# Kernel optimization log

Hardware: AMD Instinct MI355X
Metric: run time of the kernel (lower is better)

The kernel has to match this reference:

```python
import jax, jax.numpy as jnp
import numpy as np

MODES = 20
WIDTH = 64
EPS = 1e-5


def spectral_conv(x, w1, w2, m1, m2):
    # x: [B, C, H, W] real; w1, w2: [Ci, Co, m1, m2, 2] (real/imag)
    B, C, H, W = x.shape
    xf = jnp.fft.rfft2(x, norm='ortho')  # [B, C, H, W//2+1] complex
    w1c = w1[..., 0] + 1j * w1[..., 1]
    w2c = w2[..., 0] + 1j * w2[..., 1]
    m1 = min(m1, H)
    m2 = min(m2, W // 2 + 1)
    top = jnp.einsum('bixy,ioxy->boxy', xf[:, :, :m1, :m2], w1c[:, :, :m1, :m2])
    bot = jnp.einsum('bixy,ioxy->boxy', xf[:, :, -m1:, :m2], w2c[:, :, :m1, :m2])
    out = jnp.zeros((B, w1.shape[1], H, W // 2 + 1), dtype=xf.dtype)
    out = out.at[:, :, :m1, :m2].set(top)
    out = out.at[:, :, H - m1:, :m2].set(bot)
    return jnp.fft.irfft2(out, s=(H, W), norm='ortho')


def batchnorm2d(x, gamma, beta):
    # training-mode BN over (B, H, W) per channel; x: [B, C, H, W]
    mean = jnp.mean(x, axis=(0, 2, 3), keepdims=True)
    var = jnp.var(x, axis=(0, 2, 3), keepdims=True)
    xn = (x - mean) * jax.lax.rsqrt(var + EPS)
    return xn * gamma[None, :, None, None] + beta[None, :, None, None]


def setup_inputs() -> dict:
    key = jax.random.key(0)
    ks = jax.random.split(key, 12)
    B, H, W, Tin2 = 8, 256, 256, 12
    scale = 1.0 / (WIDTH * WIDTH)
    return {
        'x': jax.random.normal(ks[0], (B, H, W, Tin2), jnp.float32),
        'fc0_w': jax.random.normal(ks[1], (Tin2, WIDTH), jnp.float32) * 0.1,
        'fc0_b': jnp.zeros((WIDTH,), jnp.float32),
        'sw1': scale * jax.random.normal(ks[2], (4, WIDTH, WIDTH, MODES, MODES, 2), jnp.float32),
        'sw2': scale * jax.random.normal(ks[3], (4, WIDTH, WIDTH, MODES, MODES, 2), jnp.float32),
        'cw': jax.random.normal(ks[4], (4, WIDTH, WIDTH), jnp.float32) * 0.1,
        'cb': jnp.zeros((4, WIDTH), jnp.float32),
        'bng': jnp.ones((4, WIDTH), jnp.float32),
        'bnb': jnp.zeros((4, WIDTH), jnp.float32),
        'fc1_w': jax.random.normal(ks[5], (WIDTH, 128), jnp.float32) * 0.1,
        'fc1_b': jnp.zeros((128,), jnp.float32),
        'fc2_w': jax.random.normal(ks[6], (128, 1), jnp.float32) * 0.1,
        'fc2_b': jnp.zeros((1,), jnp.float32),
    }


def reference(x, fc0_w, fc0_b, sw1, sw2, cw, cb, bng, bnb, fc1_w, fc1_b, fc2_w, fc2_b):
    # lift: [B, H, W, Tin+2] -> [B, C, H, W]
    h = jnp.einsum('bhwt,tc->bhwc', x, fc0_w) + fc0_b
    h = jnp.transpose(h, (0, 3, 1, 2))
    for l in range(4):
        spec = spectral_conv(h, sw1[l], sw2[l], MODES, MODES)
        lin = jnp.einsum('bihw,oi->bohw', h, cw[l]) + cb[l][None, :, None, None]
        h = batchnorm2d(spec + lin, bng[l], bnb[l])
        if l < 3:
            h = jax.nn.relu(h)
    h = jnp.transpose(h, (0, 2, 3, 1))  # [B, H, W, C]
    h = jax.nn.relu(jnp.einsum('bhwc,cd->bhwd', h, fc1_w) + fc1_b)
    out = jnp.einsum('bhwd,de->bhwe', h, fc2_w) + fc2_b
    return out
```

## Files before the change

### kernel.cpp

```cpp
#include <hip/hip_runtime.h>
#include <hip/hip_bf16.h>


__device__ __forceinline__ void gll16(const float* gsrc, float* ldst) {
    __builtin_amdgcn_global_load_lds(
        (const __attribute__((address_space(1))) void*)gsrc,
        (__attribute__((address_space(3))) void*)ldst, 16, 0, 0);
}

__global__ __launch_bounds__(256) void init_k(const float* __restrict__ cw,
                                              float* __restrict__ costab, float* __restrict__ sintab,
                                              float* __restrict__ EA, float* __restrict__ Tw,
                                              float* __restrict__ cwT, float* __restrict__ stats) {
    int idx = blockIdx.x * 256 + threadIdx.x;
    const float PH = 6.28318530717958647692f / 256.f;
    if (idx < 256) {
        float s, c; sincosf(idx * PH, &s, &c);
        costab[idx] = c; sintab[idx] = s;
    } else if (idx < 256 + 10240) {
        int e = idx - 256;
        int w = e / 40, n = e % 40, ky = n >> 1;
        int r = (ky * w) & 255;
        float s, c; sincosf(r * PH, &s, &c);
        EA[e] = (n & 1) ? -s : c;
    } else if (idx < 256 + 20480) {
        int e = idx - 10496;
        int kp = e >> 8, w = e & 255;
        int ky = kp >> 1, p = kp & 1;
        int r = (ky * w) & 255;
        float s, c; sincosf(r * PH, &s, &c);
        float v;
        if (ky == 0) v = p ? 0.f : (1.f / 16.f);
        else         v = p ? (-2.f / 16.f) * s : (2.f / 16.f) * c;
        Tw[e] = v;
    } else if (idx < 256 + 20480 + 16384) {
        int e = idx - 20736;
        int l = e >> 12, r2 = e & 4095;
        int i = r2 >> 6, o = r2 & 63;
        cwT[e] = cw[(l << 12) + (o << 6) + i];
    } else if (idx < 256 + 20480 + 16384 + 2048) {
        stats[idx - 37120] = 0.f;
    }
}

__global__ __launch_bounds__(256) void wtrans_k(const float* __restrict__ sw1,
                                                const float* __restrict__ sw2,
                                                unsigned int* __restrict__ wt) {
    int gid = blockIdx.x * 4 + (threadIdx.x >> 6);
    int o = threadIdx.x & 63;
    int xyc = gid % 25;
    int i = (gid / 25) & 63;
    int t2 = gid / 1600;
    const float* src = ((t2 & 1) ? sw2 : sw1) + (t2 >> 1) * 3276800;
    const float* sp = src + ((i * 64 + o) * 400 + xyc * 16) * 2;
    unsigned int* dp = wt + (size_t)(t2 * 400 + xyc * 16) * 4096 + i * 64 + o;
#pragma unroll
    for (int j = 0; j < 16; ++j) {
        float re = sp[2 * j], im = sp[2 * j + 1];
        unsigned int ur = __float_as_uint(re), ui = __float_as_uint(im);
        ur = (ur + 0x7fffu + ((ur >> 16) & 1u)) >> 16;
        ui = (ui + 0x7fffu + ((ui >> 16) & 1u)) & 0xffff0000u;
        dp[(size_t)j * 4096] = ur | ui;
    }
}

__global__ __launch_bounds__(256) void fc0_k(const float* __restrict__ x,
                                             const float* __restrict__ w,
                                             const float* __restrict__ bias,
                                             float* __restrict__ outb) {
    __shared__ float ws[768];
    __shared__ float bs[64];
    int tid = threadIdx.x;
    for (int i = tid; i < 768; i += 256) ws[i] = w[i];
    if (tid < 64) bs[tid] = bias[tid];
    __syncthreads();
    int pix = blockIdx.x * 256 + tid;
    int b = pix >> 16, hw = pix & 65535;
    float xv[12];
#pragma unroll
    for (int t = 0; t < 12; ++t) xv[t] = x[pix * 12 + t];
    int base = (b << 22) + hw;
    for (int c = 0; c < 64; ++c) {
        float a = bs[c];
#pragma unroll
        for (int t = 0; t < 12; ++t) a += xv[t] * ws[t * 64 + c];
        outb[base + (c << 16)] = a;
    }
}

__global__ __launch_bounds__(128) void dftw_k(float* __restrict__ X,
                                              const float* __restrict__ EA,
                                              float* __restrict__ T,
                                              const float* __restrict__ statsl,
                                              const float* __restrict__ g,
                                              const float* __restrict__ bt,
                                              int fuse) {
    __shared__ __align__(16) float Xs[32 * 68];
    __shared__ float Es[32 * 40];
    int tid = threadIdx.x;
    int tm = tid >> 3, tn = tid & 7;
    int row0 = blockIdx.x << 6;
    float sc = 1.f, sh = 0.f;
    if (fuse) {
        int c = (row0 >> 8) & 63;
        float ssum = statsl[c] + statsl[128 + c] + statsl[256 + c] + statsl[384 + c];
        float ssq  = statsl[64 + c] + statsl[192 + c] + statsl[320 + c] + statsl[448 + c];
        float mean = ssum * (1.f / 524288.f);
        float var = ssq * (1.f / 524288.f) - mean * mean;
        sc = g[c] * rsqrtf(var + 1e-5f);
        sh = bt[c] - mean * sc;
    }
    float acc[4][5];
#pragma unroll
    for (int i = 0; i < 4; ++i)
#pragma unroll
        for (int j = 0; j < 5; ++j) acc[i][j] = 0.f;

#pragma unroll 1
    for (int kc = 0; kc < 256; kc += 32) {
        __syncthreads();
#pragma unroll
        for (int r = 0; r < 4; ++r) {
            int m = tm + (r << 4);
            float4 v = *(const float4*)&X[(row0 + m) * 256 + kc + (tn << 2)];
            if (fuse) {
                v.x = fmaxf(fmaf(v.x, sc, sh), 0.f);
                v.y = fmaxf(fmaf(v.y, sc, sh), 0.f);
                v.z = fmaxf(fmaf(v.z, sc, sh), 0.f);
                v.w = fmaxf(fmaf(v.w, sc, sh), 0.f);
                *(float4*)&X[(row0 + m) * 256 + kc + (tn << 2)] = v;
            }
            int kb = tn << 2;
            Xs[(kb + 0) * 68 + m] = v.x;
            Xs[(kb + 1) * 68 + m] = v.y;
            Xs[(kb + 2) * 68 + m] = v.z;
            Xs[(kb + 3) * 68 + m] = v.w;
        }
        for (int i = tid; i < 1280; i += 128) Es[i] = EA[kc * 40 + i];
        __syncthreads();
#pragma unroll 4
        for (int kk = 0; kk < 32; ++kk) {
            float4 a = *(const float4*)&Xs[kk * 68 + (tm << 2)];
#pragma unroll
            for (int j = 0; j < 5; ++j) {
                float bv = Es[kk * 40 + tn * 5 + j];
                acc[0][j] += a.x * bv;
                acc[1][j] += a.y * bv;
                acc[2][j] += a.z * bv;
                acc[3][j] += a.w * bv;
            }
        }
    }
#pragma unroll
    for (int i = 0; i < 4; ++i) {
        int row = row0 + (tm << 2) + i;
#pragma unroll
        for (int j = 0; j < 5; ++j) T[row * 40 + tn * 5 + j] = acc[i][j];
    }
}

__global__ __launch_bounds__(256) void dfth_k(const float* __restrict__ T,
                                              const float* __restrict__ ct, const float* __restrict__ st,
                                              float* __restrict__ XF) {
    __shared__ __align__(16) float Ts[10240];
    __shared__ float cts[256], sts[256];
    int tid = threadIdx.x;
    int bc = blockIdx.x;
    for (int i = tid; i < 10240; i += 256) Ts[i] = T[bc * 10240 + i];
    cts[tid] = ct[tid]; sts[tid] = st[tid];
    __syncthreads();
    if (tid < 200) {
        int kxi = tid / 5, kyg = tid % 5;
        int kxa = kxi < 20 ? kxi : kxi + 216;
        float ar0 = 0, ai0 = 0, ar1 = 0, ai1 = 0, ar2 = 0, ai2 = 0, ar3 = 0, ai3 = 0;
        int r = 0;
#pragma unroll 1
        for (int h = 0; h < 256; ++h) {
            float cc = cts[r], sv = sts[r];
            r = (r + kxa) & 255;
            float4 v0 = *(const float4*)&Ts[h * 40 + (kyg << 3)];
            float4 v1 = *(const float4*)&Ts[h * 40 + (kyg << 3) + 4];
            ar0 += v0.x * cc + v0.y * sv;  ai0 += v0.y * cc - v0.x * sv;
            ar1 += v0.z * cc + v0.w * sv;  ai1 += v0.w * cc - v0.z * sv;
            ar2 += v1.x * cc + v1.y * sv;  ai2 += v1.y * cc - v1.x * sv;
            ar3 += v1.z * cc + v1.w * sv;  ai3 += v1.w * cc - v1.z * sv;
        }
        int b = bc >> 6, c = bc & 63;
        const float s = 1.f / 256.f;
        int A = (b * 40 + kxi) * 20 + (kyg << 2);
        float2* O = (float2*)XF;
        O[(A + 0) * 64 + c] = make_float2(ar0 * s, ai0 * s);
        O[(A + 1) * 64 + c] = make_float2(ar1 * s, ai1 * s);
        O[(A + 2) * 64 + c] = make_float2(ar2 * s, ai2 * s);
        O[(A + 3) * 64 + c] = make_float2(ar3 * s, ai3 * s);
    }
}

__global__ __launch_bounds__(512) void eins_t_k(const float* __restrict__ XF,
                                                const unsigned int* __restrict__ wtl,
                                                float* __restrict__ YF) {
    __shared__ float xfs[1024];
    int tid = threadIdx.x;
    int x = blockIdx.x / 20, y = blockIdx.x % 20;
    for (int i = tid; i < 1024; i += 512) {
        int b = i >> 7, rr = i & 127;
        xfs[i] = XF[(b * 40 + x) * 2560 + y * 128 + rr];
    }
    __syncthreads();
    int b = tid >> 6, o = tid & 63;
    const unsigned int* wp = wtl + (size_t)(((x < 20 ? 0 : 400) + (x % 20) * 20 + y)) * 4096 + o;
    float ar = 0.f, ai = 0.f;
#pragma unroll 8
    for (int i = 0; i < 64; ++i) {
        unsigned int wv = wp[i << 6];
        float wr = __uint_as_float(wv << 16);
        float wi = __uint_as_float(wv & 0xffff0000u);
        float xr = xfs[(b << 7) + (i << 1)];
        float xi = xfs[(b << 7) + (i << 1) + 1];
        ar += xr * wr - xi * wi;
        ai += xr * wi + xi * wr;
    }
    ((float2*)YF)[((b * 40 + x) * 20 + y) * 64 + o] = make_float2(ar, ai);
}

__global__ __launch_bounds__(512) void eins_k(const float* __restrict__ XF,
                                              const float* __restrict__ w1, const float* __restrict__ w2,
                                              float* __restrict__ YF) {
    __shared__ float xfs[1024];
    int tid = threadIdx.x;
    int x = blockIdx.x / 20, y = blockIdx.x % 20;
    for (int i = tid; i < 1024; i += 512) {
        int b = i >> 7, rr = i & 127;
        xfs[i] = XF[(b * 40 + x) * 2560 + y * 128 + rr];
    }
    __syncthreads();
    int b = tid >> 6, o = tid & 63;
    const float* wp = (x < 20) ? (w1 + (x * 20 + y) * 2) : (w2 + ((x - 20) * 20 + y) * 2);
    float ar = 0.f, ai = 0.f;
#pragma unroll 8
    for (int i = 0; i < 64; ++i) {
        float2 wv = *(const float2*)&wp[(i * 64 + o) * 800];
        float xr = xfs[(b << 7) + (i << 1)];
        float xi = xfs[(b << 7) + (i << 1) + 1];
        ar += xr * wv.x - xi * wv.y;
        ai += xr * wv.y + xi * wv.x;
    }
    ((float2*)YF)[((b * 40 + x) * 20 + y) * 64 + o] = make_float2(ar, ai);
}

__global__ __launch_bounds__(256) void idfth_k(const float* __restrict__ YF,
                                               const float* __restrict__ ct, const float* __restrict__ st,
                                               float* __restrict__ Z) {
    __shared__ __align__(16) float yfs[1600];
    __shared__ float cts[256], sts[256];
    int tid = threadIdx.x;
    int bc = blockIdx.x;
    int b = bc >> 6, co = bc & 63;
    for (int i = tid; i < 800; i += 256) {
        int kx = i / 20, ky = i % 20;
        float2 v = ((const float2*)YF)[((b * 40 + kx) * 20 + ky) * 64 + co];
        yfs[kx * 40 + 2 * ky] = v.x;
        yfs[kx * 40 + 2 * ky + 1] = v.y;
    }
    cts[tid] = ct[tid]; sts[tid] = st[tid];
    __syncthreads();
    int h = tid;
    float accr[20], acci[20];
#pragma unroll
    for (int q = 0; q < 20; ++q) { accr[q] = 0.f; acci[q] = 0.f; }
#pragma unroll 1
    for (int kxi = 0; kxi < 40; ++kxi) {
        int kxa = kxi < 20 ? kxi : kxi + 216;
        int r = (kxa * h) & 255;
        float cc = cts[r], sv = sts[r];
#pragma unroll
        for (int q = 0; q < 10; ++q) {
            float4 v = *(const float4*)&yfs[kxi * 40 + (q << 2)];
            accr[2 * q]     += v.x * cc - v.y * sv;  acci[2 * q]     += v.x * sv + v.y * cc;
            accr[2 * q + 1] += v.z * cc - v.w * sv;  acci[2 * q + 1] += v.z * sv + v.w * cc;
        }
    }
    const float s = 1.f / 16.f;
    int base = (bc * 256 + h) * 40;
#pragma unroll
    for (int q = 0; q < 10; ++q) {
        float4 o4;
        o4.x = accr[2 * q] * s;     o4.y = acci[2 * q] * s;
        o4.z = accr[2 * q + 1] * s; o4.w = acci[2 * q + 1] * s;
        *(float4*)&Z[base + (q << 2)] = o4;
    }
}

#define FMA2(I, AV, J, B4) \
    acc[I][J].x += (AV) * B4.x; acc[I][J].y += (AV) * B4.y; \
    acc[I][J].z += (AV) * B4.z; acc[I][J].w += (AV) * B4.w;

#define FMA_COL(J, B4) \
    FMA2(0, a0.x, J, B4) FMA2(1, a0.y, J, B4) FMA2(2, a0.z, J, B4) FMA2(3, a0.w, J, B4) \
    FMA2(4, a1.x, J, B4) FMA2(5, a1.y, J, B4) FMA2(6, a1.z, J, B4) FMA2(7, a1.w, J, B4)

__global__ __launch_bounds__(256, 3) void speclin_k(const float* __restrict__ hin,
                                                    const float* __restrict__ Z,
                                                    const float* __restrict__ cwTl,
                                                    const float* __restrict__ Tw,
                                                    const float* __restrict__ cbl,
                                                    float* __restrict__ pre,
                                                    float* __restrict__ statsl) {
    __shared__ __align__(16) float AZ[104 * 68];
    __shared__ __align__(16) float Bs[2][2048];
    int tid = threadIdx.x;
    int bh = blockIdx.x;
    int b = bh >> 8, h = bh & 255;
    int to = tid >> 5, tw = tid & 31;
    int o0 = to << 3;

#pragma unroll
    for (int t = 0; t < 4; ++t) {
        int i4 = tid + (t << 8);
        float4 v = *(const float4*)&cwTl[i4 << 2];
        int row = i4 >> 4, c4 = (i4 & 15) << 2;
        float* d = &AZ[row * 68 + c4];
        d[0] = v.x; d[1] = v.y; d[2] = v.z; d[3] = v.w;
    }
    {
        const float* Zrow = Z + (size_t)(((b << 6) << 8) + h) * 40;
#pragma unroll
        for (int t = 0; t < 3; ++t) {
            int i4 = tid + (t << 8);
            if (i4 < 640) {
                int q = i4 % 10, o = i4 / 10;
                float4 v = *(const float4*)&Zrow[o * 10240 + (q << 2)];
                int rb = (64 + (q << 2)) * 68 + o;
                AZ[rb] = v.x; AZ[rb + 68] = v.y; AZ[rb + 136] = v.z; AZ[rb + 204] = v.w;
            }
        }
    }
    const float* hrow = hin + ((size_t)(((b << 6) << 8) + h) << 8);
#pragma unroll
    for (int t = 0; t < 2; ++t) {
        int i4 = tid + (t << 8);
        gll16(&hrow[((i4 >> 6) << 16) + ((i4 & 63) << 2)], &Bs[0][i4 << 2]);
    }
    __syncthreads();

    float4 acc[8][2];
#pragma unroll
    for (int i = 0; i < 8; ++i) {
        acc[i][0] = make_float4(0.f, 0.f, 0.f, 0.f);
        acc[i][1] = make_float4(0.f, 0.f, 0.f, 0.f);
    }

    int cur = 0;
#pragma unroll 1
    for (int ch = 0; ch < 13; ++ch) {
        if (ch < 12) {
            int gk0 = (ch + 1) << 3;
#pragma unroll
            for (int t = 0; t < 2; ++t) {
                int i4 = tid + (t << 8);
                int kk = i4 >> 6, w4 = (i4 & 63) << 2;
                const float* src = (gk0 < 64) ? &hrow[((gk0 + kk) << 16) + w4]
                                              : &Tw[((gk0 - 64 + kk) << 8) + w4];
                gll16(src, &Bs[cur ^ 1][i4 << 2]);
            }
        }
        const float* Bc = Bs[cur];
        const float* Ac = &AZ[(ch << 3) * 68 + o0];
#pragma unroll 2
        for (int kk = 0; kk < 8; ++kk) {
            float4 a0 = *(const float4*)&Ac[kk * 68];
            float4 a1 = *(const float4*)&Ac[kk * 68 + 4];
            float4 b0 = *(const float4*)&Bc[(kk << 8) + (tw << 2)];
            float4 b1 = *(const float4*)&Bc[(kk << 8) + 128 + (tw << 2)];
            FMA_COL(0, b0)
            FMA_COL(1, b1)
        }
        __syncthreads();
        cur ^= 1;
    }

    float* srep = statsl + ((bh & 3) << 7);
#pragma unroll
    for (int i = 0; i < 8; ++i) {
        float cbv = cbl[o0 + i];
        float sum = 0.f, sq = 0.f;
        size_t obase = ((size_t)((((b << 6) + o0 + i) << 8) + h) << 8);
#pragma unroll
        for (int j = 0; j < 2; ++j) {
            float4 v = acc[i][j];
            v.x += cbv; v.y += cbv; v.z += cbv; v.w += cbv;
            *(float4*)&pre[obase + (j << 7) + (tw << 2)] = v;
            sum += v.x + v.y + v.z + v.w;
            sq  += v.x * v.x + v.y * v.y + v.z * v.z + v.w * v.w;
        }
        sum += __shfl_xor(sum, 1);  sq += __shfl_xor(sq, 1);
        sum += __shfl_xor(sum, 2);  sq += __shfl_xor(sq, 2);
        sum += __shfl_xor(sum, 4);  sq += __shfl_xor(sq, 4);
        sum += __shfl_xor(sum, 8);  sq += __shfl_xor(sq, 8);
        sum += __shfl_xor(sum, 16); sq += __shfl_xor(sq, 16);
        if ((tid & 31) == 0) {
            atomicAdd(&srep[o0 + i], sum);
            atomicAdd(&srep[64 + o0 + i], sq);
        }
    }
}

__global__ __launch_bounds__(256, 2) void fc12_k(const float* __restrict__ hin,
                                                 const float* __restrict__ statsl,
                                                 const float* __restrict__ g,
                                                 const float* __restrict__ bt,
                                                 const float* __restrict__ w1, const float* __restrict__ b1,
                                                 const float* __restrict__ w2, const float* __restrict__ b2,
                                                 float* __restrict__ out) {
    __shared__ __align__(16) float As[64 * 128];
    __shared__ __align__(16) float Bs[2][2048];
    __shared__ float scs[64], shs[64], bias2[128];
    __shared__ __align__(16) float red[4 * 256];
    int tid = threadIdx.x;
    int bh = blockIdx.x;
    int b = bh >> 8, h = bh & 255;
    int to = tid >> 4, tw = tid & 15;
    int d0 = to << 3;

    if (tid < 64) {
        float ssum = statsl[tid] + statsl[128 + tid] + statsl[256 + tid] + statsl[384 + tid];
        float ssq  = statsl[64 + tid] + statsl[192 + tid] + statsl[320 + tid] + statsl[448 + tid];
        float mean = ssum * (1.f / 524288.f);
        float var = ssq * (1.f / 524288.f) - mean * mean;
        float s = g[tid] * rsqrtf(var + 1e-5f);
        scs[tid] = s; shs[tid] = bt[tid] - mean * s;
    }
    __syncthreads();
    for (int i = tid; i < 8192; i += 256) As[i] = w1[i] * scs[i >> 7];
    if (tid < 128) {
        float a = b1[tid];
        for (int c = 0; c < 64; ++c) a += shs[c] * w1[c * 128 + tid];
        bias2[tid] = a;
    }
    const float* hrow = hin + ((size_t)(((b << 6) << 8) + h) << 8);
#pragma unroll
    for (int t = 0; t < 2; ++t) {
        int i4 = tid + (t << 8);
        gll16(&hrow[((i4 >> 6) << 16) + ((i4 & 63) << 2)], &Bs[0][i4 << 2]);
    }
    __syncthreads();

    float4 acc[8][4];
#pragma unroll
    for (int i = 0; i < 8; ++i)
#pragma unroll
        for (int j = 0; j < 4; ++j) acc[i][j] = make_float4(0.f, 0.f, 0.f, 0.f);

    int cur = 0;
#pragma unroll 1
    for (int ch = 0; ch < 8; ++ch) {
        if (ch < 7) {
#pragma unroll
            for (int t = 0; t < 2; ++t) {
                int i4 = tid + (t << 8);
                int k = i4 >> 6, w4 = (i4 & 63) << 2;
                gll16(&hrow[((((ch + 1) << 3) + k) << 16) + w4], &Bs[cur ^ 1][i4 << 2]);
            }
        }
        const float* Bc = Bs[cur];
#pragma unroll 2
        for (int kk = 0; kk < 8; ++kk) {
            int gk = (ch << 3) + kk;
            float4 a0 = *(const float4*)&As[(gk << 7) + d0];
            float4 a1 = *(const float4*)&As[(gk << 7) + d0 + 4];
            float4 b0 = *(const float4*)&Bc[(kk << 8) + (tw << 2)];
            float4 b1 = *(const float4*)&Bc[(kk << 8) + 64 + (tw << 2)];
            FMA_COL(0, b0)
            FMA_COL(1, b1)
            float4 b2 = *(const float4*)&Bc[(kk << 8) + 128 + (tw << 2)];
            float4 b3 = *(const float4*)&Bc[(kk << 8) + 192 + (tw << 2)];
            FMA_COL(2, b2)
            FMA_COL(3, b3)
        }
        __syncthreads();
        cur ^= 1;
    }

    float bb[8], wv[8];
#pragma unroll
    for (int i = 0; i < 8; ++i) { bb[i] = bias2[d0 + i]; wv[i] = w2[d0 + i]; }
    float4 p[4];
#pragma unroll
    for (int j = 0; j < 4; ++j) {
        float4 v = make_float4(0.f, 0.f, 0.f, 0.f);
#pragma unroll
        for (int i = 0; i < 8; ++i) {
            v.x += fmaxf(acc[i][j].x + bb[i], 0.f) * wv[i];
            v.y += fmaxf(acc[i][j].y + bb[i], 0.f) * wv[i];
            v.z += fmaxf(acc[i][j].z + bb[i], 0.f) * wv[i];
            v.w += fmaxf(acc[i][j].w + bb[i], 0.f) * wv[i];
        }
        v.x += __shfl_xor(v.x, 16); v.y += __shfl_xor(v.y, 16);
        v.z += __shfl_xor(v.z, 16); v.w += __shfl_xor(v.w, 16);
        v.x += __shfl_xor(v.x, 32); v.y += __shfl_xor(v.y, 32);
        v.z += __shfl_xor(v.z, 32); v.w += __shfl_xor(v.w, 32);
        p[j] = v;
    }
    int wave = tid >> 6;
    if ((tid & 63) < 16) {
#pragma unroll
        for (int j = 0; j < 4; ++j)
            *(float4*)&red[(wave << 8) + (j << 6) + (tw << 2)] = p[j];
    }
    __syncthreads();
    float s2 = b2[0] + red[tid] + red[256 + tid] + red[512 + tid] + red[768 + tid];
    out[(b * 256 + h) * 256 + tid] = s2;
}

extern "C" void kernel_launch(void* const* d_in, const int* in_sizes, int n_in,
                              void* d_out, int out_size, void* d_ws, size_t ws_size,
                              hipStream_t stream) {
    (void)in_sizes; (void)n_in; (void)out_size;
    const float* x     = (const float*)d_in[0];
    const float* fc0_w = (const float*)d_in[1];
    const float* fc0_b = (const float*)d_in[2];
    const float* sw1   = (const float*)d_in[3];
    const float* sw2   = (const float*)d_in[4];
    const float* cw    = (const float*)d_in[5];
    const float* cb    = (const float*)d_in[6];
    const float* bng   = (const float*)d_in[7];
    const float* bnb   = (const float*)d_in[8];
    const float* fc1_w = (const float*)d_in[9];
    const float* fc1_b = (const float*)d_in[10];
    const float* fc2_w = (const float*)d_in[11];
    const float* fc2_b = (const float*)d_in[12];
    float* out = (float*)d_out;

    float* ws = (float*)d_ws;
    float* hbuf   = ws;
    float* tz     = hbuf + 33554432;
    float* xf     = tz + 5242880;
    float* yf     = xf + 819200;
    float* costab = yf + 819200;
    float* sintab = costab + 256;
    float* EA     = sintab + 256;
    float* Tw     = EA + 10240;
    float* cwT    = Tw + 10240;
    float* stats  = cwT + 16384;
    unsigned int* wt = (unsigned int*)(stats + 2048);

    size_t base_floats = 40473600 + 2048;
    int use_wt = (ws_size >= (base_floats + 13107200ull) * 4ull) ? 1 : 0;

    init_k<<<153, 256, 0, stream>>>(cw, costab, sintab, EA, Tw, cwT, stats);
    if (use_wt) wtrans_k<<<3200, 256, 0, stream>>>(sw1, sw2, wt);
    fc0_k<<<2048, 256, 0, stream>>>(x, fc0_w, fc0_b, hbuf);

    for (int l = 0; l < 4; ++l) {
        if (l == 0)
            dftw_k<<<2048, 128, 0, stream>>>(hbuf, EA, tz, stats, bng, bnb, 0);
        else
            dftw_k<<<2048, 128, 0, stream>>>(hbuf, EA, tz, stats + (l - 1) * 512,
                                             bng + (l - 1) * 64, bnb + (l - 1) * 64, 1);
        dfth_k<<<512, 256, 0, stream>>>(tz, costab, sintab, xf);
        if (use_wt)
            eins_t_k<<<800, 512, 0, stream>>>(xf, wt + (size_t)l * 2 * 400 * 4096, yf);
        else
            eins_k<<<800, 512, 0, stream>>>(xf, sw1 + l * 3276800, sw2 + l * 3276800, yf);
        idfth_k<<<512, 256, 0, stream>>>(yf, costab, sintab, tz);
        speclin_k<<<2048, 256, 0, stream>>>(hbuf, tz, cwT + l * 4096, Tw, cb + l * 64,
                                            hbuf, stats + l * 512);
    }
    fc12_k<<<2048, 256, 0, stream>>>(hbuf, stats + 3 * 512, bng + 3 * 64, bnb + 3 * 64,
                                     fc1_w, fc1_b, fc2_w, fc2_b, out);
}
```

Before: 1.298 ms.

## Process two rows per block in speclin and vectorize twiddle reads in dftw

speclin_k now covers two h rows per block (1024 blocks instead of 2048). It reuses the loaded cw weights across both rows, and the Tw twiddle tiles are shared between the two rows' Z-spectral contributions, which lowers weight and table traffic per output. The accumulator tile doubles to 8x4 float4 and the occupancy hint in launch bounds is dropped, which may raise register pressure and lower occupancy. Separately, the EA twiddle table is transposed so dftw_k can read it from LDS with float4 loads instead of scalar loads.

New measurement: 1.229 ms. -5.3%, faster.

```diff
diff --git a/kernel.cpp b/kernel.cpp
--- a/kernel.cpp
+++ b/kernel.cpp
@@ -10,7 +10,7 @@
 
 __global__ __launch_bounds__(256) void init_k(const float* __restrict__ cw,
                                               float* __restrict__ costab, float* __restrict__ sintab,
-                                              float* __restrict__ EA, float* __restrict__ Tw,
+                                              float* __restrict__ EAt, float* __restrict__ Tw,
                                               float* __restrict__ cwT, float* __restrict__ stats) {
     int idx = blockIdx.x * 256 + threadIdx.x;
     const float PH = 6.28318530717958647692f / 256.f;
@@ -19,10 +19,10 @@
         costab[idx] = c; sintab[idx] = s;
     } else if (idx < 256 + 10240) {
         int e = idx - 256;
-        int w = e / 40, n = e % 40, ky = n >> 1;
+        int n = e >> 8, w = e & 255, ky = n >> 1;
         int r = (ky * w) & 255;
         float s, c; sincosf(r * PH, &s, &c);
-        EA[e] = (n & 1) ? -s : c;
+        EAt[e] = (n & 1) ? -s : c;
     } else if (idx < 256 + 20480) {
         int e = idx - 10496;
         int kp = e >> 8, w = e & 255;
@@ -89,14 +89,14 @@
 }
 
 __global__ __launch_bounds__(128) void dftw_k(float* __restrict__ X,
-                                              const float* __restrict__ EA,
+                                              const float* __restrict__ EAt,
                                               float* __restrict__ T,
                                               const float* __restrict__ statsl,
                                               const float* __restrict__ g,
                                               const float* __restrict__ bt,
                                               int fuse) {
     __shared__ __align__(16) float Xs[32 * 68];
-    __shared__ float Es[32 * 40];
+    __shared__ __align__(16) float Est[40 * 32];
     int tid = threadIdx.x;
     int tm = tid >> 3, tn = tid & 7;
     int row0 = blockIdx.x << 6;
@@ -136,18 +136,28 @@
             Xs[(kb + 2) * 68 + m] = v.z;
             Xs[(kb + 3) * 68 + m] = v.w;
         }
-        for (int i = tid; i < 1280; i += 128) Es[i] = EA[kc * 40 + i];
+        for (int i = tid; i < 1280; i += 128) Est[i] = EAt[((i >> 5) << 8) + kc + (i & 31)];
         __syncthreads();
-#pragma unroll 4
-        for (int kk = 0; kk < 32; ++kk) {
-            float4 a = *(const float4*)&Xs[kk * 68 + (tm << 2)];
-#pragma unroll
-            for (int j = 0; j < 5; ++j) {
-                float bv = Es[kk * 40 + tn * 5 + j];
-                acc[0][j] += a.x * bv;
-                acc[1][j] += a.y * bv;
-                acc[2][j] += a.z * bv;
-                acc[3][j] += a.w * bv;
+#pragma unroll 1
+        for (int k4 = 0; k4 < 8; ++k4) {
+            float4 e0 = *(const float4*)&Est[(tn * 5 + 0) * 32 + (k4 << 2)];
+            float4 e1 = *(const float4*)&Est[(tn * 5 + 1) * 32 + (k4 << 2)];
+            float4 e2 = *(const float4*)&Est[(tn * 5 + 2) * 32 + (k4 << 2)];
+            float4 e3 = *(const float4*)&Est[(tn * 5 + 3) * 32 + (k4 << 2)];
+            float4 e4 = *(const float4*)&Est[(tn * 5 + 4) * 32 + (k4 << 2)];
+#pragma unroll
+            for (int c2 = 0; c2 < 4; ++c2) {
+                float4 a = *(const float4*)&Xs[((k4 << 2) + c2) * 68 + (tm << 2)];
+                float ev0 = ((const float*)&e0)[c2];
+                float ev1 = ((const float*)&e1)[c2];
+                float ev2 = ((const float*)&e2)[c2];
+                float ev3 = ((const float*)&e3)[c2];
+                float ev4 = ((const float*)&e4)[c2];
+                acc[0][0] += a.x * ev0; acc[1][0] += a.y * ev0; acc[2][0] += a.z * ev0; acc[3][0] += a.w * ev0;
+                acc[0][1] += a.x * ev1; acc[1][1] += a.y * ev1; acc[2][1] += a.z * ev1; acc[3][1] += a.w * ev1;
+                acc[0][2] += a.x * ev2; acc[1][2] += a.y * ev2; acc[2][2] += a.z * ev2; acc[3][2] += a.w * ev2;
+                acc[0][3] += a.x * ev3; acc[1][3] += a.y * ev3; acc[2][3] += a.z * ev3; acc[3][3] += a.w * ev3;
+                acc[0][4] += a.x * ev4; acc[1][4] += a.y * ev4; acc[2][4] += a.z * ev4; acc[3][4] += a.w * ev4;
             }
         }
     }
@@ -299,18 +309,28 @@
     FMA2(0, a0.x, J, B4) FMA2(1, a0.y, J, B4) FMA2(2, a0.z, J, B4) FMA2(3, a0.w, J, B4) \
     FMA2(4, a1.x, J, B4) FMA2(5, a1.y, J, B4) FMA2(6, a1.z, J, B4) FMA2(7, a1.w, J, B4)
 
-__global__ __launch_bounds__(256, 3) void speclin_k(const float* __restrict__ hin,
-                                                    const float* __restrict__ Z,
-                                                    const float* __restrict__ cwTl,
-                                                    const float* __restrict__ Tw,
-                                                    const float* __restrict__ cbl,
-                                                    float* __restrict__ pre,
-                                                    float* __restrict__ statsl) {
-    __shared__ __align__(16) float AZ[104 * 68];
-    __shared__ __align__(16) float Bs[2][2048];
-    int tid = threadIdx.x;
-    int bh = blockIdx.x;
-    int b = bh >> 8, h = bh & 255;
+#define FMA_COLU(J, B4) \
+    FMA2(0, au0.x, J, B4) FMA2(1, au0.y, J, B4) FMA2(2, au0.z, J, B4) FMA2(3, au0.w, J, B4) \
+    FMA2(4, au1.x, J, B4) FMA2(5, au1.y, J, B4) FMA2(6, au1.z, J, B4) FMA2(7, au1.w, J, B4)
+
+#define FMA_COLD(J, B4) \
+    FMA2(0, ad0.x, J, B4) FMA2(1, ad0.y, J, B4) FMA2(2, ad0.z, J, B4) FMA2(3, ad0.w, J, B4) \
+    FMA2(4, ad1.x, J, B4) FMA2(5, ad1.y, J, B4) FMA2(6, ad1.z, J, B4) FMA2(7, ad1.w, J, B4)
+
+__global__ __launch_bounds__(256) void speclin_k(const float* __restrict__ hin,
+                                                 const float* __restrict__ Z,
+                                                 const float* __restrict__ cwTl,
+                                                 const float* __restrict__ Tw,
+                                                 const float* __restrict__ cbl,
+                                                 float* __restrict__ pre,
+                                                 float* __restrict__ statsl) {
+    __shared__ __align__(16) float As[64 * 68];
+    __shared__ __align__(16) float Zs[80 * 64];
+    __shared__ __align__(16) float Bs[2][4096];
+    int tid = threadIdx.x;
+    int bid = blockIdx.x;
+    int b = bid >> 7, hp = bid & 127;
+    int h0 = hp << 1;
     int to = tid >> 5, tw = tid & 31;
     int o0 = to << 3;
 
@@ -318,78 +338,114 @@
     for (int t = 0; t < 4; ++t) {
         int i4 = tid + (t << 8);
         float4 v = *(const float4*)&cwTl[i4 << 2];
-        int row = i4 >> 4, c4 = (i4 & 15) << 2;
-        float* d = &AZ[row * 68 + c4];
+        float* d = &As[(i4 >> 4) * 68 + ((i4 & 15) << 2)];
         d[0] = v.x; d[1] = v.y; d[2] = v.z; d[3] = v.w;
     }
-    {
-        const float* Zrow = Z + (size_t)(((b << 6) << 8) + h) * 40;
-#pragma unroll
-        for (int t = 0; t < 3; ++t) {
-            int i4 = tid + (t << 8);
-            if (i4 < 640) {
-                int q = i4 % 10, o = i4 / 10;
-                float4 v = *(const float4*)&Zrow[o * 10240 + (q << 2)];
-                int rb = (64 + (q << 2)) * 68 + o;
-                AZ[rb] = v.x; AZ[rb + 68] = v.y; AZ[rb + 136] = v.z; AZ[rb + 204] = v.w;
+#pragma unroll
+    for (int t = 0; t < 5; ++t) {
+        int i4 = tid + (t << 8);
+        int q = i4 % 10;
+        int u = i4 / 10;
+        int o = u & 63, r = u >> 6;
+        float4 v = *(const float4*)&Z[(((b << 6) + o) * 256 + h0 + r) * 40 + (q << 2)];
+        int base = ((r * 40 + (q << 2)) << 6) + o;
+        Zs[base]       = v.x;
+        Zs[base + 64]  = v.y;
+        Zs[base + 128] = v.z;
+        Zs[base + 192] = v.w;
+    }
+    const float* hrow = hin + (size_t)((((b << 6) << 8) + h0) << 8);
+#pragma unroll
+    for (int t = 0; t < 4; ++t) {
+        int i4 = tid + (t << 8);
+        int k = i4 >> 7, n4 = i4 & 127, r = n4 >> 6, w4 = n4 & 63;
+        gll16(&hrow[(k << 16) + (r << 8) + (w4 << 2)], &Bs[0][i4 << 2]);
+    }
+    __syncthreads();
+
+    float4 acc[8][4];
+#pragma unroll
+    for (int i = 0; i < 8; ++i)
+#pragma unroll
+        for (int j = 0; j < 4; ++j) acc[i][j] = make_float4(0.f, 0.f, 0.f, 0.f);
+
+    int cur = 0;
+#pragma unroll 1
+    for (int ch = 0; ch < 8; ++ch) {
+        if (ch < 7) {
+#pragma unroll
+            for (int t = 0; t < 4; ++t) {
+                int i4 = tid + (t << 8);
+                int k = i4 >> 7, n4 = i4 & 127, r = n4 >> 6, w4 = n4 & 63;
+                gll16(&hrow[((((ch + 1) << 3) + k) << 16) + (r << 8) + (w4 << 2)],
+                      &Bs[cur ^ 1][i4 << 2]);
             }
-        }
-    }
-    const float* hrow = hin + ((size_t)(((b << 6) << 8) + h) << 8);
-#pragma unroll
-    for (int t = 0; t < 2; ++t) {
-        int i4 = tid + (t << 8);
-        gll16(&hrow[((i4 >> 6) << 16) + ((i4 & 63) << 2)], &Bs[0][i4 << 2]);
-    }
-    __syncthreads();
-
-    float4 acc[8][2];
-#pragma unroll
-    for (int i = 0; i < 8; ++i) {
-        acc[i][0] = make_float4(0.f, 0.f, 0.f, 0.f);
-        acc[i][1] = make_float4(0.f, 0.f, 0.f, 0.f);
-    }
-
-    int cur = 0;
-#pragma unroll 1
-    for (int ch = 0; ch < 13; ++ch) {
-        if (ch < 12) {
-            int gk0 = (ch + 1) << 3;
+        } else {
 #pragma unroll
             for (int t = 0; t < 2; ++t) {
                 int i4 = tid + (t << 8);
-                int kk = i4 >> 6, w4 = (i4 & 63) << 2;
-                const float* src = (gk0 < 64) ? &hrow[((gk0 + kk) << 16) + w4]
-                                              : &Tw[((gk0 - 64 + kk) << 8) + w4];
-                gll16(src, &Bs[cur ^ 1][i4 << 2]);
+                gll16(&Tw[i4 << 2], &Bs[cur ^ 1][i4 << 2]);
             }
         }
         const float* Bc = Bs[cur];
-        const float* Ac = &AZ[(ch << 3) * 68 + o0];
-#pragma unroll 2
+        const float* Ac = &As[(ch << 3) * 68 + o0];
+#pragma unroll 1
         for (int kk = 0; kk < 8; ++kk) {
             float4 a0 = *(const float4*)&Ac[kk * 68];
             float4 a1 = *(const float4*)&Ac[kk * 68 + 4];
+            float4 b0 = *(const float4*)&Bc[(kk << 9) + (tw << 2)];
+            float4 b1 = *(const float4*)&Bc[(kk << 9) + 128 + (tw << 2)];
+            FMA_COL(0, b0)
+            FMA_COL(1, b1)
+            float4 b2 = *(const float4*)&Bc[(kk << 9) + 256 + (tw << 2)];
+            float4 b3 = *(const float4*)&Bc[(kk << 9) + 384 + (tw << 2)];
+            FMA_COL(2, b2)
+            FMA_COL(3, b3)
+        }
+        __syncthreads();
+        cur ^= 1;
+    }
+
+#pragma unroll 1
+    for (int ch = 0; ch < 5; ++ch) {
+        if (ch < 4) {
+#pragma unroll
+            for (int t = 0; t < 2; ++t) {
+                int i4 = tid + (t << 8);
+                gll16(&Tw[(((ch + 1) << 3) << 8) + (i4 << 2)], &Bs[cur ^ 1][i4 << 2]);
+            }
+        }
+        const float* Bc = Bs[cur];
+#pragma unroll 1
+        for (int kk = 0; kk < 8; ++kk) {
+            int kp = (ch << 3) + kk;
             float4 b0 = *(const float4*)&Bc[(kk << 8) + (tw << 2)];
             float4 b1 = *(const float4*)&Bc[(kk << 8) + 128 + (tw << 2)];
-            FMA_COL(0, b0)
-            FMA_COL(1, b1)
+            float4 au0 = *(const float4*)&Zs[(kp << 6) + o0];
+            float4 au1 = *(const float4*)&Zs[(kp << 6) + o0 + 4];
+            FMA_COLU(0, b0)
+            FMA_COLU(1, b1)
+            float4 ad0 = *(const float4*)&Zs[((40 + kp) << 6) + o0];
+            float4 ad1 = *(const float4*)&Zs[((40 + kp) << 6) + o0 + 4];
+            FMA_COLD(2, b0)
+            FMA_COLD(3, b1)
         }
         __syncthreads();
         cur ^= 1;
     }
 
-    float* srep = statsl + ((bh & 3) << 7);
+    float* srep = statsl + ((bid & 3) << 7);
 #pragma unroll
     for (int i = 0; i < 8; ++i) {
         float cbv = cbl[o0 + i];
         float sum = 0.f, sq = 0.f;
-        size_t obase = ((size_t)((((b << 6) + o0 + i) << 8) + h) << 8);
-#pragma unroll
-        for (int j = 0; j < 2; ++j) {
+#pragma unroll
+        for (int j = 0; j < 4; ++j) {
             float4 v = acc[i][j];
             v.x += cbv; v.y += cbv; v.z += cbv; v.w += cbv;
-            *(float4*)&pre[obase + (j << 7) + (tw << 2)] = v;
+            int row = h0 + (j >> 1);
+            int wc = ((j & 1) << 7) + (tw << 2);
+            *(float4*)&pre[(size_t)((((b << 6) + o0 + i) << 8) + row) * 256 + wc] = v;
             sum += v.x + v.y + v.z + v.w;
             sq  += v.x * v.x + v.y * v.y + v.z * v.z + v.w * v.w;
         }
@@ -538,8 +594,8 @@
     float* yf     = xf + 819200;
     float* costab = yf + 819200;
     float* sintab = costab + 256;
-    float* EA     = sintab + 256;
-    float* Tw     = EA + 10240;
+    float* EAt    = sintab + 256;
+    float* Tw     = EAt + 10240;
     float* cwT    = Tw + 10240;
     float* stats  = cwT + 16384;
     unsigned int* wt = (unsigned int*)(stats + 2048);
@@ -547,15 +603,15 @@
     size_t base_floats = 40473600 + 2048;
     int use_wt = (ws_size >= (base_floats + 13107200ull) * 4ull) ? 1 : 0;
 
-    init_k<<<153, 256, 0, stream>>>(cw, costab, sintab, EA, Tw, cwT, stats);
+    init_k<<<153, 256, 0, stream>>>(cw, costab, sintab, EAt, Tw, cwT, stats);
     if (use_wt) wtrans_k<<<3200, 256, 0, stream>>>(sw1, sw2, wt);
     fc0_k<<<2048, 256, 0, stream>>>(x, fc0_w, fc0_b, hbuf);
 
     for (int l = 0; l < 4; ++l) {
         if (l == 0)
-            dftw_k<<<2048, 128, 0, stream>>>(hbuf, EA, tz, stats, bng, bnb, 0);
+            dftw_k<<<2048, 128, 0, stream>>>(hbuf, EAt, tz, stats, bng, bnb, 0);
         else
-            dftw_k<<<2048, 128, 0, stream>>>(hbuf, EA, tz, stats + (l - 1) * 512,
+            dftw_k<<<2048, 128, 0, stream>>>(hbuf, EAt, tz, stats + (l - 1) * 512,
                                              bng + (l - 1) * 64, bnb + (l - 1) * 64, 1);
         dfth_k<<<512, 256, 0, stream>>>(tz, costab, sintab, xf);
         if (use_wt)
@@ -563,7 +619,7 @@
         else
             eins_k<<<800, 512, 0, stream>>>(xf, sw1 + l * 3276800, sw2 + l * 3276800, yf);
         idfth_k<<<512, 256, 0, stream>>>(yf, costab, sintab, tz);
-        speclin_k<<<2048, 256, 0, stream>>>(hbuf, tz, cwT + l * 4096, Tw, cb + l * 64,
+        speclin_k<<<1024, 256, 0, stream>>>(hbuf, tz, cwT + l * 4096, Tw, cb + l * 64,
                                             hbuf, stats + l * 512);
     }
     fc12_k<<<2048, 256, 0, stream>>>(hbuf, stats + 3 * 512, bng + 3 * 64, bnb + 3 * 64,
```
